# Kernel optimization log

Measured on AMD Instinct MI355X. Metric: run time of the kernel, lower is better.

The kernel has to match this reference:

```python
import jax, jax.numpy as jnp
import numpy as np

B, S, T = 16384, 64, 64
I, M, H = 4, 16, 64  # input_dim, middle_dim, hidden_dim


def _cell(x, h, c, Wih, Whh, b):
    # PyTorch LSTM cell, gate order i, f, g, o; b = b_ih + b_hh
    gates = x @ Wih.T + h @ Whh.T + b
    i, f, g, o = jnp.split(gates, 4, axis=-1)
    c = jax.nn.sigmoid(f) * c + jax.nn.sigmoid(i) * jnp.tanh(g)
    h = jax.nn.sigmoid(o) * jnp.tanh(c)
    return h, c


def setup_inputs() -> dict:
    key = jax.random.key(0)
    ks = jax.random.split(key, 18)
    p = lambda k, shape: (jax.random.uniform(k, shape, jnp.float32) - 0.5) * 0.25
    return {
        "src": jax.random.normal(ks[0], (B, S, I), jnp.float32),
        "trg": jax.random.normal(ks[1], (B, T, I), jnp.float32),
        "W_in": p(ks[2], (M, I)), "b_in": p(ks[3], (M,)),
        "enc_Wih0": p(ks[4], (4 * H, M)), "enc_Whh0": p(ks[5], (4 * H, H)), "enc_b0": p(ks[6], (4 * H,)),
        "enc_Wih1": p(ks[7], (4 * H, H)), "enc_Whh1": p(ks[8], (4 * H, H)), "enc_b1": p(ks[9], (4 * H,)),
        "dec_Wih0": p(ks[10], (4 * H, M)), "dec_Whh0": p(ks[11], (4 * H, H)), "dec_b0": p(ks[12], (4 * H,)),
        "dec_Wih1": p(ks[13], (4 * H, H)), "dec_Whh1": p(ks[14], (4 * H, H)), "dec_b1": p(ks[15], (4 * H,)),
        "W_out": p(ks[16], (I, H)), "b_out": p(ks[17], (I,)),
    }


def reference(src, trg, W_in, b_in,
              enc_Wih0, enc_Whh0, enc_b0, enc_Wih1, enc_Whh1, enc_b1,
              dec_Wih0, dec_Whh0, dec_b0, dec_Wih1, dec_Whh1, dec_b1,
              W_out, b_out):
    b = src.shape[0]
    dt = src.dtype

    def layer_scan(xs, Wih, Whh, bb):
        # xs: [S, B, D] -> ys: [S, B, H], final (h, c)
        h0 = jnp.zeros((b, H), dt)
        def step(carry, x):
            h, c = carry
            h, c = _cell(x, h, c, Wih, Whh, bb)
            return (h, c), h
        (h, c), ys = jax.lax.scan(step, (h0, h0), xs)
        return ys, h, c

    # encoder: fc_in then 2-layer LSTM (dropout inactive in eval)
    mid = src @ W_in.T + b_in                      # [B, S, M]
    ys1, h1, c1 = layer_scan(mid.transpose(1, 0, 2), enc_Wih0, enc_Whh0, enc_b0)
    _, h2, c2 = layer_scan(ys1, enc_Wih1, enc_Whh1, enc_b1)

    # stepwise decoder, teacher_forcing_ratio=0 branch: next input = pred + trg[:, t-1]
    def dec_step(carry, trg_t):
        h1, c1, h2, c2, x = carry
        m = x @ W_in.T + b_in                      # [B, M]
        h1, c1 = _cell(m, h1, c1, dec_Wih0, dec_Whh0, dec_b0)
        h2, c2 = _cell(h1, h2, c2, dec_Wih1, dec_Whh1, dec_b1)
        pred = h2 @ W_out.T + b_out                # [B, I]
        return (h1, c1, h2, c2, pred + trg_t), pred

    init = (h1, c1, h2, c2, trg[:, 0])
    _, preds = jax.lax.scan(dec_step, init, trg.transpose(1, 0, 2))  # [T, B, I]
    return preds.transpose(1, 0, 2) + trg
```

## Files before the change

### kernel.cpp

```cpp
#include <hip/hip_runtime.h>

typedef __bf16 bf16x8 __attribute__((ext_vector_type(8)));
typedef float  f32x4  __attribute__((ext_vector_type(4)));

__device__ __forceinline__ unsigned short f2bf(float x){
  return __builtin_bit_cast(unsigned short, (__bf16)x);
}

__global__ void pack_weights(const float* __restrict__ eWih0, const float* __restrict__ eWhh0,
                             const float* __restrict__ eWih1, const float* __restrict__ eWhh1,
                             const float* __restrict__ dWih0, const float* __restrict__ dWhh0,
                             const float* __restrict__ dWih1, const float* __restrict__ dWhh1,
                             const float* __restrict__ Wout,
                             unsigned short* __restrict__ out){
  int t = blockIdx.x * 256 + threadIdx.x;
  if (t >= 226 * 64) return;
  int lane = t & 63;
  int f    = t >> 6;
  unsigned short vals[8];
  if (f >= 224){
    int kt = f - 224, n = lane & 15;
#pragma unroll
    for (int jj = 0; jj < 8; jj++){
      int k = kt * 32 + (lane >> 4) * 8 + jj;
      vals[jj] = (n < 4) ? f2bf(Wout[n * 64 + k]) : (unsigned short)0;
    }
  } else {
    const float *Wih, *Whh; int kx, ntile, kt;
    if (f < 48)       { Wih=eWih0; Whh=eWhh0; kx=16; ntile=f/3;        kt=f%3; }
    else if (f < 112) { Wih=eWih1; Whh=eWhh1; kx=64; ntile=(f-48)/4;   kt=(f-48)%4; }
    else if (f < 160) { Wih=dWih0; Whh=dWhh0; kx=16; ntile=(f-112)/3;  kt=(f-112)%3; }
    else              { Wih=dWih1; Whh=dWhh1; kx=64; ntile=(f-160)/4;  kt=(f-160)%4; }
    int n    = ntile * 16 + (lane & 15);
    int hoff = (kx == 16) ? 32 : 64;
    float scale = ((ntile >> 2) == 2) ? -2.88539008f : -1.44269504f;
#pragma unroll
    for (int jj = 0; jj < 8; jj++){
      int k = kt * 32 + (lane >> 4) * 8 + jj;
      float v;
      if (k < kx)        v = Wih[n * kx + k];
      else if (k < hoff) v = 0.0f;
      else               v = Whh[n * 64 + (k - hoff)];
      vals[jj] = f2bf(v * scale);
    }
  }
  uint4 o;
  o.x = (unsigned)vals[0] | ((unsigned)vals[1] << 16);
  o.y = (unsigned)vals[2] | ((unsigned)vals[3] << 16);
  o.z = (unsigned)vals[4] | ((unsigned)vals[5] << 16);
  o.w = (unsigned)vals[6] | ((unsigned)vals[7] << 16);
  ((uint4*)out)[f * 64 + lane] = o;
}

__device__ __forceinline__ void write_h(unsigned short* buf, int k, int quad,
                                        const unsigned short* h){
  unsigned short* p = buf + (((k >> 5) * 64) + quad * 4 + (((k >> 3) & 3) << 4)) * 8 + (k & 7);
#pragma unroll
  for (int e = 0; e < 4; e++) p[e * 8] = h[e];
}

__device__ __forceinline__ void load_frags(const unsigned short* __restrict__ pw,
                                           int base0, int base1, int w, int lane,
                                           bf16x8 (&B0)[3][4], bf16x8 (&B1)[4][4]){
#pragma unroll
  for (int g = 0; g < 4; g++){
    int nt = 4 * g + w;
#pragma unroll
    for (int kt = 0; kt < 3; kt++)
      B0[kt][g] = *(const bf16x8*)(pw + (((long)(base0 + nt * 3 + kt)) * 64 + lane) * 8);
#pragma unroll
    for (int kt = 0; kt < 4; kt++)
      B1[kt][g] = *(const bf16x8*)(pw + (((long)(base1 + nt * 4 + kt)) * 64 + lane) * 8);
  }
}

template<int KT, int SZ>
__device__ __forceinline__ void cell_compute(const unsigned short* __restrict__ A,
                                             const bf16x8 (&B)[KT][4],
                                             const float (&bias)[4],
                                             float (&c)[8],
                                             unsigned short (&hout)[8],
                                             int lane){
  f32x4 acc[4][2];
#pragma unroll
  for (int g = 0; g < 4; g++){
    f32x4 b = {bias[g], bias[g], bias[g], bias[g]};
    acc[g][0] = b; acc[g][1] = b;
  }
#pragma unroll
  for (int kt = 0; kt < KT; kt++){
    bf16x8 a0 = *(const bf16x8*)(A +      (kt * 64 + lane) * 8);
    bf16x8 a1 = *(const bf16x8*)(A + SZ + (kt * 64 + lane) * 8);
#pragma unroll
    for (int g = 0; g < 4; g++){
      acc[g][0] = __builtin_amdgcn_mfma_f32_16x16x32_bf16(a0, B[kt][g], acc[g][0], 0, 0, 0);
      acc[g][1] = __builtin_amdgcn_mfma_f32_16x16x32_bf16(a1, B[kt][g], acc[g][1], 0, 0, 0);
    }
  }
#pragma unroll
  for (int rt = 0; rt < 2; rt++){
#pragma unroll
    for (int e = 0; e < 4; e++){
      int idx = rt * 4 + e;
      float ei = __builtin_amdgcn_exp2f(acc[0][rt][e]);
      float ef = __builtin_amdgcn_exp2f(acc[1][rt][e]);
      float eg = __builtin_amdgcn_exp2f(acc[2][rt][e]);
      float eo = __builtin_amdgcn_exp2f(acc[3][rt][e]);
      float rf  = __builtin_amdgcn_rcpf(1.0f + ef);
      float rig = __builtin_amdgcn_rcpf((1.0f + ei) * (1.0f + eg));
      float c2  = fmaf(c[idx], rf, fmaf(-2.88539008f, eg, 2.88539008f) * rig);
      c[idx] = c2;
      float ec  = __builtin_amdgcn_exp2f(c2);
      float rot = __builtin_amdgcn_rcpf((1.0f + eo) * (1.0f + ec));
      hout[idx] = f2bf((ec - 1.0f) * rot);
    }
  }
}

__global__ __launch_bounds__(256, 2)
void lstm_main(const float* __restrict__ src, const float* __restrict__ trg,
               const float* __restrict__ W_in, const float* __restrict__ b_in,
               const float* __restrict__ eb0, const float* __restrict__ eb1,
               const float* __restrict__ db0, const float* __restrict__ db1,
               const float* __restrict__ bout,
               const unsigned short* __restrict__ pw,
               float* __restrict__ out){
  __shared__ __align__(16) unsigned short A0[2][2][1536];
  __shared__ __align__(16) unsigned short A1[2][2][2048];
  __shared__ __align__(16) float xsrc[2][128];
  __shared__ __align__(16) float xfb[128];
  __shared__ __align__(16) unsigned short sWoutF[1024];

  const int tid  = threadIdx.x;
  const int lane = tid & 63;
  const int w    = tid >> 6;
  const int quad = lane >> 4;
  const int l16  = lane & 15;
  const int j    = 16 * w + l16;
  const int rowg0 = blockIdx.x * 32;
  const int mm   = tid & 15;
  const int xr   = tid >> 4;

  {
    uint4 z; z.x = z.y = z.z = z.w = 0u;
    uint4* a0p = (uint4*)A0;
    uint4* a1p = (uint4*)A1;
    for (int i = tid; i < 768;  i += 256) a0p[i] = z;
    for (int i = tid; i < 1024; i += 256) a1p[i] = z;
    if (tid < 128) ((uint4*)sWoutF)[tid] = ((const uint4*)pw)[224 * 64 + tid];
    if (tid < 128) xsrc[0][tid] = src[(long)(rowg0 + (tid >> 2)) * 256 + (tid & 3)];
  }
  const float4 wv = *(const float4*)&W_in[mm * 4];
  const float  bin = b_in[mm];

  bf16x8 B0[3][4], B1[4][4];
  float bias0[4], bias1[4];
  float c0[8] = {0,0,0,0,0,0,0,0}, c1[8] = {0,0,0,0,0,0,0,0};
  load_frags(pw, 0, 48, w, lane, B0, B1);
#pragma unroll
  for (int g = 0; g < 4; g++){
    int n = 64*g + j;
    float s = (g == 2) ? -2.88539008f : -1.44269504f;
    bias0[g] = eb0[n] * s; bias1[g] = eb1[n] * s;
  }
  __syncthreads();

  unsigned short h0r[8], h1r[8];
  const int xoff = (xr | ((mm >> 3) << 4)) * 8 + (mm & 7);

  for (int t = 0; t < 64; t++){
    int cur = t & 1, nxt = cur ^ 1;
    float xv;
    if (tid < 128)
      xv = src[(long)(rowg0 + (tid >> 2)) * 256 + ((t == 63 ? 63 : t + 1) << 2) + (tid & 3)];
    {
      float4 x0 = *(const float4*)&xsrc[cur][xr * 4];
      float4 x1 = *(const float4*)&xsrc[cur][(xr + 16) * 4];
      float m0 = bin + x0.x*wv.x + x0.y*wv.y + x0.z*wv.z + x0.w*wv.w;
      float m1 = bin + x1.x*wv.x + x1.y*wv.y + x1.z*wv.z + x1.w*wv.w;
      A0[cur][0][xoff] = f2bf(m0);
      A0[cur][1][xoff] = f2bf(m1);
    }
    if (tid < 128) xsrc[nxt][tid] = xv;
    __syncthreads();
    cell_compute<3, 1536>(&A0[cur][0][0], B0, bias0, c0, h0r, lane);
#pragma unroll
    for (int rt = 0; rt < 2; rt++){
      write_h(&A0[nxt][rt][0], 32 + j, quad, h0r + rt * 4);
      write_h(&A1[cur][rt][0],      j, quad, h0r + rt * 4);
    }
    if (t > 0){
      cell_compute<4, 2048>(&A1[nxt][0][0], B1, bias1, c1, h1r, lane);
#pragma unroll
      for (int rt = 0; rt < 2; rt++)
        write_h(&A1[cur][rt][0], 64 + j, quad, h1r + rt * 4);
    }
  }
  __syncthreads();
  cell_compute<4, 2048>(&A1[1][0][0], B1, bias1, c1, h1r, lane);
#pragma unroll
  for (int rt = 0; rt < 2; rt++)
    write_h(&A1[0][rt][0], 64 + j, quad, h1r + rt * 4);

  load_frags(pw, 112, 160, w, lane, B0, B1);
#pragma unroll
  for (int g = 0; g < 4; g++){
    int n = 64*g + j;
    float s = (g == 2) ? -2.88539008f : -1.44269504f;
    bias0[g] = db0[n] * s; bias1[g] = db1[n] * s;
  }
  const float bo = (w < 2 && l16 < 4) ? bout[l16] : 0.0f;
  if (tid < 128) xfb[tid] = trg[(long)(rowg0 + (tid >> 2)) * 256 + (tid & 3)];
  __syncthreads();

  for (int t = 0; t < 64; t++){
    int cur = t & 1, nxt = cur ^ 1;
    float tpre[4];
    if (w < 2 && l16 < 4){
#pragma unroll
      for (int e = 0; e < 4; e++)
        tpre[e] = trg[(long)(rowg0 + w * 16 + quad * 4 + e) * 256 + t * 4 + l16];
    }
    {
      float4 x0 = *(const float4*)&xfb[xr * 4];
      float4 x1 = *(const float4*)&xfb[(xr + 16) * 4];
      float m0 = bin + x0.x*wv.x + x0.y*wv.y + x0.z*wv.z + x0.w*wv.w;
      float m1 = bin + x1.x*wv.x + x1.y*wv.y + x1.z*wv.z + x1.w*wv.w;
      A0[cur][0][xoff] = f2bf(m0);
      A0[cur][1][xoff] = f2bf(m1);
    }
    __syncthreads();
    cell_compute<3, 1536>(&A0[cur][0][0], B0, bias0, c0, h0r, lane);
#pragma unroll
    for (int rt = 0; rt < 2; rt++){
      write_h(&A0[nxt][rt][0], 32 + j, quad, h0r + rt * 4);
      write_h(&A1[cur][rt][0],      j, quad, h0r + rt * 4);
    }
    __syncthreads();
    cell_compute<4, 2048>(&A1[cur][0][0], B1, bias1, c1, h1r, lane);
#pragma unroll
    for (int rt = 0; rt < 2; rt++)
      write_h(&A1[nxt][rt][0], 64 + j, quad, h1r + rt * 4);
    __syncthreads();
    if (w < 2){
      const unsigned short* Ah = &A1[nxt][w][0];
      bf16x8 a2 = *(const bf16x8*)(Ah + (2 * 64 + lane) * 8);
      bf16x8 a3 = *(const bf16x8*)(Ah + (3 * 64 + lane) * 8);
      bf16x8 bw0 = *(const bf16x8*)(sWoutF + lane * 8);
      bf16x8 bw1 = *(const bf16x8*)(sWoutF + 512 + lane * 8);
      f32x4 po = {bo, bo, bo, bo};
      po = __builtin_amdgcn_mfma_f32_16x16x32_bf16(a2, bw0, po, 0, 0, 0);
      po = __builtin_amdgcn_mfma_f32_16x16x32_bf16(a3, bw1, po, 0, 0, 0);
      if (l16 < 4){
#pragma unroll
        for (int e = 0; e < 4; e++){
          int row = w * 16 + quad * 4 + e;
          float v = po[e] + tpre[e];
          out[(long)(rowg0 + row) * 256 + t * 4 + l16] = v;
          xfb[row * 4 + l16] = v;
        }
      }
    }
    __syncthreads();
  }
}

extern "C" void kernel_launch(void* const* d_in, const int* in_sizes, int n_in,
                              void* d_out, int out_size, void* d_ws, size_t ws_size,
                              hipStream_t stream){
  (void)n_in; (void)out_size; (void)ws_size;
  const float* src   = (const float*)d_in[0];
  const float* trg   = (const float*)d_in[1];
  const float* W_in  = (const float*)d_in[2];
  const float* b_in  = (const float*)d_in[3];
  const float* eWih0 = (const float*)d_in[4];
  const float* eWhh0 = (const float*)d_in[5];
  const float* eb0   = (const float*)d_in[6];
  const float* eWih1 = (const float*)d_in[7];
  const float* eWhh1 = (const float*)d_in[8];
  const float* eb1   = (const float*)d_in[9];
  const float* dWih0 = (const float*)d_in[10];
  const float* dWhh0 = (const float*)d_in[11];
  const float* db0   = (const float*)d_in[12];
  const float* dWih1 = (const float*)d_in[13];
  const float* dWhh1 = (const float*)d_in[14];
  const float* db1   = (const float*)d_in[15];
  const float* Wout  = (const float*)d_in[16];
  const float* bout  = (const float*)d_in[17];
  unsigned short* pw = (unsigned short*)d_ws;

  pack_weights<<<57, 256, 0, stream>>>(eWih0, eWhh0, eWih1, eWhh1,
                                       dWih0, dWhh0, dWih1, dWhh1, Wout, pw);

  int B    = in_sizes[0] / 256;
  int nblk = B / 32;
  lstm_main<<<nblk, 256, 0, stream>>>(src, trg, W_in, b_in, eb0, eb1, db0, db1,
                                      bout, pw, (float*)d_out);
}
```

Measured before the change: 453.4 us.

## Fold output projection into decoder layer-0 weights to drop a per-step barrier

```diff
diff --git a/kernel.cpp b/kernel.cpp
--- a/kernel.cpp
+++ b/kernel.cpp
@@ -11,26 +11,26 @@
                              const float* __restrict__ eWih1, const float* __restrict__ eWhh1,
                              const float* __restrict__ dWih0, const float* __restrict__ dWhh0,
                              const float* __restrict__ dWih1, const float* __restrict__ dWhh1,
-                             const float* __restrict__ Wout,
+                             const float* __restrict__ Wout,  const float* __restrict__ W_in,
                              unsigned short* __restrict__ out){
   int t = blockIdx.x * 256 + threadIdx.x;
-  if (t >= 226 * 64) return;
+  if (t >= 258 * 64) return;
   int lane = t & 63;
   int f    = t >> 6;
   unsigned short vals[8];
-  if (f >= 224){
-    int kt = f - 224, n = lane & 15;
+  if (f >= 256){
+    int kt = f - 256, n = lane & 15;
 #pragma unroll
     for (int jj = 0; jj < 8; jj++){
       int k = kt * 32 + (lane >> 4) * 8 + jj;
       vals[jj] = (n < 4) ? f2bf(Wout[n * 64 + k]) : (unsigned short)0;
     }
   } else {
-    const float *Wih, *Whh; int kx, ntile, kt;
-    if (f < 48)       { Wih=eWih0; Whh=eWhh0; kx=16; ntile=f/3;        kt=f%3; }
-    else if (f < 112) { Wih=eWih1; Whh=eWhh1; kx=64; ntile=(f-48)/4;   kt=(f-48)%4; }
-    else if (f < 160) { Wih=dWih0; Whh=dWhh0; kx=16; ntile=(f-112)/3;  kt=(f-112)%3; }
-    else              { Wih=dWih1; Whh=dWhh1; kx=64; ntile=(f-160)/4;  kt=(f-160)%4; }
+    const float *Wih, *Whh; int kx, ntile, kt, nkt;
+    if (f < 48)       { Wih=eWih0; Whh=eWhh0; kx=16; nkt=3; ntile=f/3;        kt=f%3; }
+    else if (f < 112) { Wih=eWih1; Whh=eWhh1; kx=64; nkt=4; ntile=(f-48)/4;   kt=(f-48)%4; }
+    else if (f < 192) { Wih=dWih0; Whh=dWhh0; kx=16; nkt=5; ntile=(f-112)/5;  kt=(f-112)%5; }
+    else              { Wih=dWih1; Whh=dWhh1; kx=64; nkt=4; ntile=(f-192)/4;  kt=(f-192)%4; }
     int n    = ntile * 16 + (lane & 15);
     int hoff = (kx == 16) ? 32 : 64;
     float scale = ((ntile >> 2) == 2) ? -2.88539008f : -1.44269504f;
@@ -38,7 +38,17 @@
     for (int jj = 0; jj < 8; jj++){
       int k = kt * 32 + (lane >> 4) * 8 + jj;
       float v;
-      if (k < kx)        v = Wih[n * kx + k];
+      if (nkt == 5 && k >= 96){
+        int c = k - 96;
+        float acc = 0.0f;
+        for (int m = 0; m < 16; m++){
+          float wf = 0.0f;
+          for (int i = 0; i < 4; i++) wf += W_in[m * 4 + i] * Wout[i * 64 + c];
+          acc += Wih[n * 16 + m] * wf;
+        }
+        v = acc;
+      }
+      else if (k < kx)   v = Wih[n * kx + k];
       else if (k < hoff) v = 0.0f;
       else               v = Whh[n * 64 + (k - hoff)];
       vals[jj] = f2bf(v * scale);
@@ -59,15 +69,16 @@
   for (int e = 0; e < 4; e++) p[e * 8] = h[e];
 }
 
+template<int NKT0>
 __device__ __forceinline__ void load_frags(const unsigned short* __restrict__ pw,
                                            int base0, int base1, int w, int lane,
-                                           bf16x8 (&B0)[3][4], bf16x8 (&B1)[4][4]){
+                                           bf16x8 (&B0)[5][4], bf16x8 (&B1)[4][4]){
 #pragma unroll
   for (int g = 0; g < 4; g++){
     int nt = 4 * g + w;
 #pragma unroll
-    for (int kt = 0; kt < 3; kt++)
-      B0[kt][g] = *(const bf16x8*)(pw + (((long)(base0 + nt * 3 + kt)) * 64 + lane) * 8);
+    for (int kt = 0; kt < NKT0; kt++)
+      B0[kt][g] = *(const bf16x8*)(pw + (((long)(base0 + nt * NKT0 + kt)) * 64 + lane) * 8);
 #pragma unroll
     for (int kt = 0; kt < 4; kt++)
       B1[kt][g] = *(const bf16x8*)(pw + (((long)(base1 + nt * 4 + kt)) * 64 + lane) * 8);
@@ -76,7 +87,7 @@
 
 template<int KT, int SZ>
 __device__ __forceinline__ void cell_compute(const unsigned short* __restrict__ A,
-                                             const bf16x8 (&B)[KT][4],
+                                             const bf16x8 (*B)[4],
                                              const float (&bias)[4],
                                              float (&c)[8],
                                              unsigned short (&hout)[8],
@@ -125,10 +136,9 @@
                const float* __restrict__ bout,
                const unsigned short* __restrict__ pw,
                float* __restrict__ out){
-  __shared__ __align__(16) unsigned short A0[2][2][1536];
+  __shared__ __align__(16) unsigned short A0[2][2][2560];
   __shared__ __align__(16) unsigned short A1[2][2][2048];
   __shared__ __align__(16) float xsrc[2][128];
-  __shared__ __align__(16) float xfb[128];
   __shared__ __align__(16) unsigned short sWoutF[1024];
 
   const int tid  = threadIdx.x;
@@ -145,18 +155,18 @@
     uint4 z; z.x = z.y = z.z = z.w = 0u;
     uint4* a0p = (uint4*)A0;
     uint4* a1p = (uint4*)A1;
-    for (int i = tid; i < 768;  i += 256) a0p[i] = z;
+    for (int i = tid; i < 1280; i += 256) a0p[i] = z;
     for (int i = tid; i < 1024; i += 256) a1p[i] = z;
-    if (tid < 128) ((uint4*)sWoutF)[tid] = ((const uint4*)pw)[224 * 64 + tid];
+    if (tid < 128) ((uint4*)sWoutF)[tid] = ((const uint4*)pw)[256 * 64 + tid];
     if (tid < 128) xsrc[0][tid] = src[(long)(rowg0 + (tid >> 2)) * 256 + (tid & 3)];
   }
   const float4 wv = *(const float4*)&W_in[mm * 4];
   const float  bin = b_in[mm];
 
-  bf16x8 B0[3][4], B1[4][4];
+  bf16x8 B0[5][4], B1[4][4];
   float bias0[4], bias1[4];
   float c0[8] = {0,0,0,0,0,0,0,0}, c1[8] = {0,0,0,0,0,0,0,0};
-  load_frags(pw, 0, 48, w, lane, B0, B1);
+  load_frags<3>(pw, 0, 48, w, lane, B0, B1);
 #pragma unroll
   for (int g = 0; g < 4; g++){
     int n = 64*g + j;
@@ -183,7 +193,7 @@
     }
     if (tid < 128) xsrc[nxt][tid] = xv;
     __syncthreads();
-    cell_compute<3, 1536>(&A0[cur][0][0], B0, bias0, c0, h0r, lane);
+    cell_compute<3, 2560>(&A0[cur][0][0], B0, bias0, c0, h0r, lane);
 #pragma unroll
     for (int rt = 0; rt < 2; rt++){
       write_h(&A0[nxt][rt][0], 32 + j, quad, h0r + rt * 4);
@@ -202,35 +212,54 @@
   for (int rt = 0; rt < 2; rt++)
     write_h(&A1[0][rt][0], 64 + j, quad, h1r + rt * 4);
 
-  load_frags(pw, 112, 160, w, lane, B0, B1);
+  load_frags<5>(pw, 112, 192, w, lane, B0, B1);
 #pragma unroll
   for (int g = 0; g < 4; g++){
     int n = 64*g + j;
     float s = (g == 2) ? -2.88539008f : -1.44269504f;
     bias0[g] = db0[n] * s; bias1[g] = db1[n] * s;
   }
-  const float bo = (w < 2 && l16 < 4) ? bout[l16] : 0.0f;
-  if (tid < 128) xfb[tid] = trg[(long)(rowg0 + (tid >> 2)) * 256 + (tid & 3)];
+  const float4 bt4 = *(const float4*)bout;
+  const float  cb  = bin + wv.x*bt4.x + wv.y*bt4.y + wv.z*bt4.z + wv.w*bt4.w;
+  const float  bo  = (w < 2 && l16 < 4) ? bout[l16] : 0.0f;
+  {
+    float4 x0 = *(const float4*)&trg[(long)(rowg0 + xr) * 256];
+    float4 x1 = *(const float4*)&trg[(long)(rowg0 + xr + 16) * 256];
+    float m0 = bin + x0.x*wv.x + x0.y*wv.y + x0.z*wv.z + x0.w*wv.w;
+    float m1 = bin + x1.x*wv.x + x1.y*wv.y + x1.z*wv.z + x1.w*wv.w;
+    A0[0][0][xoff] = f2bf(m0);
+    A0[0][1][xoff] = f2bf(m1);
+  }
   __syncthreads();
 
   for (int t = 0; t < 64; t++){
     int cur = t & 1, nxt = cur ^ 1;
-    float tpre[4];
-    if (w < 2 && l16 < 4){
-#pragma unroll
-      for (int e = 0; e < 4; e++)
-        tpre[e] = trg[(long)(rowg0 + w * 16 + quad * 4 + e) * 256 + t * 4 + l16];
-    }
     {
-      float4 x0 = *(const float4*)&xfb[xr * 4];
-      float4 x1 = *(const float4*)&xfb[(xr + 16) * 4];
-      float m0 = bin + x0.x*wv.x + x0.y*wv.y + x0.z*wv.z + x0.w*wv.w;
-      float m1 = bin + x1.x*wv.x + x1.y*wv.y + x1.z*wv.z + x1.w*wv.w;
-      A0[cur][0][xoff] = f2bf(m0);
-      A0[cur][1][xoff] = f2bf(m1);
-    }
-    __syncthreads();
-    cell_compute<3, 1536>(&A0[cur][0][0], B0, bias0, c0, h0r, lane);
+      float4 x0 = *(const float4*)&trg[(long)(rowg0 + xr) * 256 + t * 4];
+      float4 x1 = *(const float4*)&trg[(long)(rowg0 + xr + 16) * 256 + t * 4];
+      float m0 = cb + x0.x*wv.x + x0.y*wv.y + x0.z*wv.z + x0.w*wv.w;
+      float m1 = cb + x1.x*wv.x + x1.y*wv.y + x1.z*wv.z + x1.w*wv.w;
+      A0[nxt][0][xoff] = f2bf(m0);
+      A0[nxt][1][xoff] = f2bf(m1);
+    }
+    if (w < 2 && t > 0){
+      const unsigned short* Ah = &A0[cur][w][0];
+      bf16x8 a3  = *(const bf16x8*)(Ah + (3 * 64 + lane) * 8);
+      bf16x8 a4  = *(const bf16x8*)(Ah + (4 * 64 + lane) * 8);
+      bf16x8 bw0 = *(const bf16x8*)(sWoutF + lane * 8);
+      bf16x8 bw1 = *(const bf16x8*)(sWoutF + 512 + lane * 8);
+      f32x4 po = {bo, bo, bo, bo};
+      po = __builtin_amdgcn_mfma_f32_16x16x32_bf16(a3, bw0, po, 0, 0, 0);
+      po = __builtin_amdgcn_mfma_f32_16x16x32_bf16(a4, bw1, po, 0, 0, 0);
+      if (l16 < 4){
+#pragma unroll
+        for (int e = 0; e < 4; e++){
+          long idx = (long)(rowg0 + w * 16 + quad * 4 + e) * 256 + (t - 1) * 4 + l16;
+          out[idx] = po[e] + trg[idx];
+        }
+      }
+    }
+    cell_compute<5, 2560>(&A0[cur][0][0], B0, bias0, c0, h0r, lane);
 #pragma unroll
     for (int rt = 0; rt < 2; rt++){
       write_h(&A0[nxt][rt][0], 32 + j, quad, h0r + rt * 4);
@@ -239,29 +268,28 @@
     __syncthreads();
     cell_compute<4, 2048>(&A1[cur][0][0], B1, bias1, c1, h1r, lane);
 #pragma unroll
-    for (int rt = 0; rt < 2; rt++)
+    for (int rt = 0; rt < 2; rt++){
       write_h(&A1[nxt][rt][0], 64 + j, quad, h1r + rt * 4);
+      write_h(&A0[nxt][rt][0], 96 + j, quad, h1r + rt * 4);
+    }
     __syncthreads();
-    if (w < 2){
-      const unsigned short* Ah = &A1[nxt][w][0];
-      bf16x8 a2 = *(const bf16x8*)(Ah + (2 * 64 + lane) * 8);
-      bf16x8 a3 = *(const bf16x8*)(Ah + (3 * 64 + lane) * 8);
-      bf16x8 bw0 = *(const bf16x8*)(sWoutF + lane * 8);
-      bf16x8 bw1 = *(const bf16x8*)(sWoutF + 512 + lane * 8);
-      f32x4 po = {bo, bo, bo, bo};
-      po = __builtin_amdgcn_mfma_f32_16x16x32_bf16(a2, bw0, po, 0, 0, 0);
-      po = __builtin_amdgcn_mfma_f32_16x16x32_bf16(a3, bw1, po, 0, 0, 0);
-      if (l16 < 4){
-#pragma unroll
-        for (int e = 0; e < 4; e++){
-          int row = w * 16 + quad * 4 + e;
-          float v = po[e] + tpre[e];
-          out[(long)(rowg0 + row) * 256 + t * 4 + l16] = v;
-          xfb[row * 4 + l16] = v;
-        }
+  }
+  if (w < 2){
+    const unsigned short* Ah = &A0[0][w][0];
+    bf16x8 a3  = *(const bf16x8*)(Ah + (3 * 64 + lane) * 8);
+    bf16x8 a4  = *(const bf16x8*)(Ah + (4 * 64 + lane) * 8);
+    bf16x8 bw0 = *(const bf16x8*)(sWoutF + lane * 8);
+    bf16x8 bw1 = *(const bf16x8*)(sWoutF + 512 + lane * 8);
+    f32x4 po = {bo, bo, bo, bo};
+    po = __builtin_amdgcn_mfma_f32_16x16x32_bf16(a3, bw0, po, 0, 0, 0);
+    po = __builtin_amdgcn_mfma_f32_16x16x32_bf16(a4, bw1, po, 0, 0, 0);
+    if (l16 < 4){
+#pragma unroll
+      for (int e = 0; e < 4; e++){
+        long idx = (long)(rowg0 + w * 16 + quad * 4 + e) * 256 + 63 * 4 + l16;
+        out[idx] = po[e] + trg[idx];
       }
     }
-    __syncthreads();
   }
 }
 
@@ -289,8 +317,8 @@
   const float* bout  = (const float*)d_in[17];
   unsigned short* pw = (unsigned short*)d_ws;
 
-  pack_weights<<<57, 256, 0, stream>>>(eWih0, eWhh0, eWih1, eWhh1,
-                                       dWih0, dWhh0, dWih1, dWhh1, Wout, pw);
+  pack_weights<<<65, 256, 0, stream>>>(eWih0, eWhh0, eWih1, eWhh1,
+                                       dWih0, dWhh0, dWih1, dWhh1, Wout, W_in, pw);
 
   int B    = in_sizes[0] / 256;
   int nblk = B / 32;
```

Result: slower. 504.0 us (+11.2%).
